# Optimization experiments

Measured on AMD Instinct MI355X. Metric: run time of the kernel, lower is better.

## Reference

```python
import jax, jax.numpy as jnp
import numpy as np

B, S, D = 16, 2048, 1024   # batch, src_len, per-tensor feature dim (input_dim*growth_factor)
OUT = 1024                 # output_dim


def setup_inputs() -> dict:
    key = jax.random.key(0)
    k1, k2, k3, k4, k5, k6 = jax.random.split(key, 6)
    hidden = jax.random.normal(k1, (B, S, D), dtype=jnp.float32)
    encoder_outputs = jax.random.normal(k2, (B, S, D), dtype=jnp.float32)
    c_t = jax.random.normal(k3, (B, D), dtype=jnp.float32)
    # Linear(input_dim*3*growth_factor=3*D, OUT): PyTorch stores weight as [OUT, 3D]
    limit = 1.0 / np.sqrt(3 * D)
    W = jax.random.uniform(k4, (OUT, 3 * D), minval=-limit, maxval=limit, dtype=jnp.float32)
    b = jax.random.uniform(k5, (OUT,), minval=-limit, maxval=limit, dtype=jnp.float32)
    v = jax.random.uniform(k6, (OUT,), dtype=jnp.float32)  # torch.rand -> U[0,1)
    return {"hidden": hidden, "encoder_outputs": encoder_outputs, "c_t": c_t,
            "W": W, "b": b, "v": v}


def reference(hidden, encoder_outputs, c_t, W, b, v):
    # c_t broadcast over src_len; concat on feature dim -> [B, S, 3D]
    c_rep = jnp.broadcast_to(c_t[:, None, :], hidden.shape)
    cat = jnp.concatenate((hidden, c_rep, encoder_outputs), axis=2)
    # energy = relu(cat @ W^T + b): [B, S, OUT]
    energy = jax.nn.relu(jnp.einsum('bsf,of->bso', cat, W) + b)
    # attention = energy @ v: [B, S], then softmax over src_len
    attention = jnp.einsum('bso,o->bs', energy, v)
    return jax.nn.softmax(attention, axis=1)
```

## Files before the change

### kernel.cpp

```cpp
#include <hip/hip_runtime.h>
#include <hip/hip_bf16.h>


typedef __attribute__((ext_vector_type(8))) short short8;
typedef __attribute__((ext_vector_type(4))) float f32x4;
typedef __attribute__((ext_vector_type(8))) unsigned short ushort8v;
typedef __attribute__((ext_vector_type(4))) unsigned short ushort4v;

#define NB 16
#define NS 2048
#define ND 1024
#define NOUT 1024
#define NM (NB * NS)
#define KHE 2048
#define TM 128
#define TN 128
#define BK 32

__device__ __forceinline__ unsigned short bf16_rne(float x) {
    unsigned int u = __float_as_uint(x);
    unsigned int r = (u + 0x7fffu + ((u >> 16) & 1u)) >> 16;
    return (unsigned short)r;
}

__device__ __forceinline__ void gload_lds16(const unsigned short* g, unsigned short* l) {
    __builtin_amdgcn_global_load_lds(
        (const __attribute__((address_space(1))) void*)g,
        (__attribute__((address_space(3))) void*)l, 16, 0, 0);
}

__global__ __launch_bounds__(256) void aconv_k(const float* __restrict__ hidden,
                                               const float* __restrict__ enc,
                                               unsigned short* __restrict__ Abf) {
    size_t c = (size_t)blockIdx.x * 256 + threadIdx.x;
    size_t m = c >> 8;
    int k = (int)(c & 255) * 8;
    const float* src = (k < ND) ? (hidden + m * ND + k) : (enc + m * ND + (k - ND));
    float4 f0 = *(const float4*)src;
    float4 f1 = *(const float4*)(src + 4);
    ushort8v h;
    h[0] = bf16_rne(f0.x); h[1] = bf16_rne(f0.y); h[2] = bf16_rne(f0.z); h[3] = bf16_rne(f0.w);
    h[4] = bf16_rne(f1.x); h[5] = bf16_rne(f1.y); h[6] = bf16_rne(f1.z); h[7] = bf16_rne(f1.w);
    *(ushort8v*)(Abf + m * KHE + k) = h;
}

__global__ __launch_bounds__(256) void wconv_k(const float* __restrict__ W,
                                               unsigned short* __restrict__ Wbf) {
    int idx = blockIdx.x * 256 + threadIdx.x;
    int o = idx >> 9;
    int k = (idx & 511) * 4;
    int off = (k < ND) ? k : (k + ND);
    float4 f = *(const float4*)(W + (size_t)o * 3072 + off);
    ushort4v h;
    h.x = bf16_rne(f.x); h.y = bf16_rne(f.y); h.z = bf16_rne(f.z); h.w = bf16_rne(f.w);
    *(ushort4v*)(Wbf + (size_t)o * KHE + k) = h;
}

__global__ __launch_bounds__(256) void cbias_k(const float* __restrict__ c_t,
                                               const float* __restrict__ W,
                                               const float* __restrict__ bias,
                                               float* __restrict__ cbias) {
    int o = blockIdx.x * 4 + (threadIdx.x >> 6);
    int lane = threadIdx.x & 63;
    const float* w = W + (size_t)o * 3072 + ND;
    float wr[16];
    #pragma unroll
    for (int j = 0; j < 16; ++j) wr[j] = w[lane + j * 64];
    float bo = bias[o];
    for (int b = 0; b < NB; ++b) {
        const float* c = c_t + (size_t)b * ND;
        float s = 0.f;
        #pragma unroll
        for (int j = 0; j < 16; ++j) s = fmaf(c[lane + j * 64], wr[j], s);
        #pragma unroll
        for (int m = 1; m < 64; m <<= 1) s += __shfl_xor(s, m);
        if (lane == 0) cbias[b * NOUT + o] = s + bo;
    }
}

__global__ __launch_bounds__(256) void gemm_att_bf_k(const unsigned short* __restrict__ Abf,
                                                     const unsigned short* __restrict__ Wbf,
                                                     const float* __restrict__ cbias,
                                                     const float* __restrict__ v,
                                                     float* __restrict__ logits) {
    __shared__ unsigned short As[TM * BK] __attribute__((aligned(16)));
    __shared__ unsigned short Bs[TN * BK] __attribute__((aligned(16)));
    __shared__ float rowsum[2][TM];
    __shared__ float cb_s[TN];
    __shared__ float v_s[TN];

    const int tid = threadIdx.x;
    const int ntile = blockIdx.x & 7;
    const int mtile = blockIdx.x >> 3;
    const int m0 = mtile * TM;
    const int o0 = ntile * TN;
    const int batch = m0 >> 11;

    if (tid < TN) {
        cb_s[tid] = cbias[batch * NOUT + o0 + tid];
        v_s[tid] = v[o0 + tid];
    }

    const int wid = tid >> 6;
    const int lane = tid & 63;
    const int wm = (wid & 1) * 64;
    const int wn = (wid >> 1) * 64;

    const int srow = lane >> 2;
    const int scol = (lane & 3) * 8;
    const unsigned short* ag0 = Abf + (size_t)(m0 + wid * 32 + srow) * KHE + scol;
    const unsigned short* ag1 = ag0 + (size_t)16 * KHE;
    const unsigned short* bg0 = Wbf + (size_t)(o0 + wid * 32 + srow) * KHE + scol;
    const unsigned short* bg1 = bg0 + (size_t)16 * KHE;
    unsigned short* al0 = As + (wid * 32) * BK;
    unsigned short* al1 = As + (wid * 32 + 16) * BK;
    unsigned short* bl0 = Bs + (wid * 32) * BK;
    unsigned short* bl1 = Bs + (wid * 32 + 16) * BK;

    f32x4 acc[4][4] = {};

    for (int kt = 0; kt < KHE; kt += BK) {
        gload_lds16(ag0 + kt, al0);
        gload_lds16(ag1 + kt, al1);
        gload_lds16(bg0 + kt, bl0);
        gload_lds16(bg1 + kt, bl1);
        __syncthreads();

        short8 a_frag[4], b_frag[4];
        #pragma unroll
        for (int i = 0; i < 4; ++i)
            a_frag[i] = *(const short8*)(As + (wm + i * 16 + (lane & 15)) * BK + (lane >> 4) * 8);
        #pragma unroll
        for (int j = 0; j < 4; ++j)
            b_frag[j] = *(const short8*)(Bs + (wn + j * 16 + (lane & 15)) * BK + (lane >> 4) * 8);
        #pragma unroll
        for (int i = 0; i < 4; ++i)
            #pragma unroll
            for (int j = 0; j < 4; ++j)
                acc[i][j] = __builtin_amdgcn_mfma_f32_16x16x32_bf16(a_frag[i], b_frag[j],
                                                                    acc[i][j], 0, 0, 0);
        __syncthreads();
    }

    const int col = lane & 15;
    const int q = lane >> 4;
    float vv[4], cbv[4];
    #pragma unroll
    for (int j = 0; j < 4; ++j) {
        int oc = wn + j * 16 + col;
        vv[j] = v_s[oc];
        cbv[j] = cb_s[oc];
    }
    #pragma unroll
    for (int i = 0; i < 4; ++i) {
        #pragma unroll
        for (int r = 0; r < 4; ++r) {
            float s = 0.f;
            #pragma unroll
            for (int j = 0; j < 4; ++j) {
                float e = acc[i][j][r] + cbv[j];
                e = fmaxf(e, 0.f);
                s = fmaf(e, vv[j], s);
            }
            s += __shfl_xor(s, 1);
            s += __shfl_xor(s, 2);
            s += __shfl_xor(s, 4);
            s += __shfl_xor(s, 8);
            if (col == 0) rowsum[wid >> 1][wm + i * 16 + q * 4 + r] = s;
        }
    }
    __syncthreads();
    if (tid < TM) atomicAdd(&logits[m0 + tid], rowsum[0][tid] + rowsum[1][tid]);
}

__global__ __launch_bounds__(256) void gemm_att_k(const float* __restrict__ hidden,
                                                  const float* __restrict__ enc,
                                                  const unsigned short* __restrict__ Wbf,
                                                  const float* __restrict__ Wf,
                                                  const float* __restrict__ cbias,
                                                  const float* __restrict__ v,
                                                  float* __restrict__ logits,
                                                  int use_wbf) {
    __shared__ unsigned short As[TM * BK] __attribute__((aligned(16)));
    __shared__ unsigned short Bs[TN * BK] __attribute__((aligned(16)));
    __shared__ float rowsum[2][TM];
    __shared__ float cb_s[TN];
    __shared__ float v_s[TN];

    const int tid = threadIdx.x;
    const int ntile = blockIdx.x & 7;
    const int mtile = blockIdx.x >> 3;
    const int m0 = mtile * TM;
    const int o0 = ntile * TN;
    const int batch = m0 >> 11;

    if (tid < TN) {
        cb_s[tid] = cbias[batch * NOUT + o0 + tid];
        v_s[tid] = v[o0 + tid];
    }

    const int wid = tid >> 6;
    const int lane = tid & 63;
    const int wm = (wid & 1) * 64;
    const int wn = (wid >> 1) * 64;

    f32x4 acc[4][4] = {};

    for (int kt = 0; kt < KHE; kt += BK) {
        const float* Abase = (kt < ND) ? hidden : enc;
        const int aoff = (kt < ND) ? kt : (kt - ND);
        #pragma unroll
        for (int i = 0; i < 4; ++i) {
            int p = tid + i * 256;
            int row = p >> 3, kc = p & 7;
            float4 f = *(const float4*)(Abase + (size_t)(m0 + row) * ND + aoff + kc * 4);
            ushort4v h;
            h.x = bf16_rne(f.x); h.y = bf16_rne(f.y); h.z = bf16_rne(f.z); h.w = bf16_rne(f.w);
            *(ushort4v*)(As + row * BK + kc * 4) = h;
        }
        if (use_wbf) {
            #pragma unroll
            for (int i = 0; i < 2; ++i) {
                int u = tid + i * 256;
                int ol = u >> 2, kc = u & 3;
                ushort8v w8 = *(const ushort8v*)(Wbf + (size_t)(o0 + ol) * KHE + kt + kc * 8);
                *(ushort8v*)(Bs + ol * BK + kc * 8) = w8;
            }
        } else {
            const int woff = (kt < ND) ? kt : (kt + ND);
            #pragma unroll
            for (int i = 0; i < 4; ++i) {
                int p = tid + i * 256;
                int row = p >> 3, kc = p & 7;
                float4 f = *(const float4*)(Wf + (size_t)(o0 + row) * 3072 + woff + kc * 4);
                ushort4v h;
                h.x = bf16_rne(f.x); h.y = bf16_rne(f.y); h.z = bf16_rne(f.z); h.w = bf16_rne(f.w);
                *(ushort4v*)(Bs + row * BK + kc * 4) = h;
            }
        }
        __syncthreads();

        short8 a_frag[4], b_frag[4];
        #pragma unroll
        for (int i = 0; i < 4; ++i)
            a_frag[i] = *(const short8*)(As + (wm + i * 16 + (lane & 15)) * BK + (lane >> 4) * 8);
        #pragma unroll
        for (int j = 0; j < 4; ++j)
            b_frag[j] = *(const short8*)(Bs + (wn + j * 16 + (lane & 15)) * BK + (lane >> 4) * 8);
        #pragma unroll
        for (int i = 0; i < 4; ++i)
            #pragma unroll
            for (int j = 0; j < 4; ++j)
                acc[i][j] = __builtin_amdgcn_mfma_f32_16x16x32_bf16(a_frag[i], b_frag[j],
                                                                    acc[i][j], 0, 0, 0);
        __syncthreads();
    }

    const int col = lane & 15;
    const int q = lane >> 4;
    float vv[4], cbv[4];
    #pragma unroll
    for (int j = 0; j < 4; ++j) {
        int oc = wn + j * 16 + col;
        vv[j] = v_s[oc];
        cbv[j] = cb_s[oc];
    }
    #pragma unroll
    for (int i = 0; i < 4; ++i) {
        #pragma unroll
        for (int r = 0; r < 4; ++r) {
            float s = 0.f;
            #pragma unroll
            for (int j = 0; j < 4; ++j) {
                float e = acc[i][j][r] + cbv[j];
                e = fmaxf(e, 0.f);
                s = fmaf(e, vv[j], s);
            }
            s += __shfl_xor(s, 1);
            s += __shfl_xor(s, 2);
            s += __shfl_xor(s, 4);
            s += __shfl_xor(s, 8);
            if (col == 0) rowsum[wid >> 1][wm + i * 16 + q * 4 + r] = s;
        }
    }
    __syncthreads();
    if (tid < TM) atomicAdd(&logits[m0 + tid], rowsum[0][tid] + rowsum[1][tid]);
}

__global__ __launch_bounds__(256) void softmax_k(const float* __restrict__ logits,
                                                 float* __restrict__ out) {
    const int b = blockIdx.x;
    const int tid = threadIdx.x;
    const int lane = tid & 63, wid = tid >> 6;
    __shared__ float redmax[4];
    __shared__ float redsum[4];
    const float* L = logits + (size_t)b * NS;
    float x[8];
    float mx = -3.4e38f;
    #pragma unroll
    for (int i = 0; i < 8; ++i) {
        x[i] = L[tid + i * 256];
        mx = fmaxf(mx, x[i]);
    }
    #pragma unroll
    for (int m = 1; m < 64; m <<= 1) mx = fmaxf(mx, __shfl_xor(mx, m));
    if (lane == 0) redmax[wid] = mx;
    __syncthreads();
    mx = fmaxf(fmaxf(redmax[0], redmax[1]), fmaxf(redmax[2], redmax[3]));
    float sum = 0.f;
    #pragma unroll
    for (int i = 0; i < 8; ++i) {
        x[i] = expf(x[i] - mx);
        sum += x[i];
    }
    #pragma unroll
    for (int m = 1; m < 64; m <<= 1) sum += __shfl_xor(sum, m);
    if (lane == 0) redsum[wid] = sum;
    __syncthreads();
    float inv = 1.0f / (redsum[0] + redsum[1] + redsum[2] + redsum[3]);
    #pragma unroll
    for (int i = 0; i < 8; ++i) out[(size_t)b * NS + tid + i * 256] = x[i] * inv;
}

extern "C" void kernel_launch(void* const* d_in, const int* in_sizes, int n_in,
                              void* d_out, int out_size, void* d_ws, size_t ws_size,
                              hipStream_t stream) {
    const float* hidden = (const float*)d_in[0];
    const float* enc    = (const float*)d_in[1];
    const float* c_t    = (const float*)d_in[2];
    const float* W      = (const float*)d_in[3];
    const float* bias   = (const float*)d_in[4];
    const float* v      = (const float*)d_in[5];
    float* out = (float*)d_out;

    char* ws = (char*)d_ws;
    float* logits = (float*)ws;
    float* cbias  = (float*)(ws + 131072);
    unsigned short* Wbf = (unsigned short*)(ws + 196608);
    unsigned short* Abf = (unsigned short*)(ws + 196608 + 4194304);
    const size_t need_wbf = 196608 + (size_t)NOUT * KHE * 2;
    const size_t need_abf = need_wbf + (size_t)NM * KHE * 2;

    hipMemsetAsync(logits, 0, NM * sizeof(float), stream);
    cbias_k<<<NOUT / 4, 256, 0, stream>>>(c_t, W, bias, cbias);

    if (ws_size >= need_abf) {
        wconv_k<<<(NOUT * KHE / 4) / 256, 256, 0, stream>>>(W, Wbf);
        aconv_k<<<(int)(((size_t)NM * KHE / 8) / 256), 256, 0, stream>>>(hidden, enc, Abf);
        gemm_att_bf_k<<<(NM / TM) * (NOUT / TN), 256, 0, stream>>>(Abf, Wbf, cbias, v, logits);
    } else if (ws_size >= need_wbf) {
        wconv_k<<<(NOUT * KHE / 4) / 256, 256, 0, stream>>>(W, Wbf);
        gemm_att_k<<<(NM / TM) * (NOUT / TN), 256, 0, stream>>>(hidden, enc, Wbf, W, cbias, v,
                                                                logits, 1);
    } else {
        gemm_att_k<<<(NM / TM) * (NOUT / TN), 256, 0, stream>>>(hidden, enc, Wbf, W, cbias, v,
                                                                logits, 0);
    }
    softmax_k<<<NB, 256, 0, stream>>>(logits, out);
}
```

Baseline: 495.1 us.

## Fuse prep kernels and double K-tile with XOR-swizzled LDS layout in bf16 GEMM

Merges the memset, c_t bias, weight and activation conversions into a single prep kernel to cut launch overhead. The bf16 GEMM moves from a 32-wide to a 64-wide K tile, which halves the number of barrier pairs per tile. Its LDS layout is XOR-swizzled by row so fragment reads avoid bank conflicts. The larger tile doubles LDS use per block, which may lower occupancy.

```diff
diff --git a/kernel.cpp b/kernel.cpp
--- a/kernel.cpp
+++ b/kernel.cpp
@@ -15,7 +15,12 @@
 #define KHE 2048
 #define TM 128
 #define TN 128
-#define BK 32
+#define BK 64
+
+#define PREP_ACONV 16384
+#define PREP_WCONV 2048
+#define PREP_CBIAS 256
+#define PREP_ZERO 32
 
 __device__ __forceinline__ unsigned short bf16_rne(float x) {
     unsigned int u = __float_as_uint(x);
@@ -29,19 +34,63 @@
         (__attribute__((address_space(3))) void*)l, 16, 0, 0);
 }
 
-__global__ __launch_bounds__(256) void aconv_k(const float* __restrict__ hidden,
-                                               const float* __restrict__ enc,
-                                               unsigned short* __restrict__ Abf) {
-    size_t c = (size_t)blockIdx.x * 256 + threadIdx.x;
-    size_t m = c >> 8;
-    int k = (int)(c & 255) * 8;
-    const float* src = (k < ND) ? (hidden + m * ND + k) : (enc + m * ND + (k - ND));
-    float4 f0 = *(const float4*)src;
-    float4 f1 = *(const float4*)(src + 4);
-    ushort8v h;
-    h[0] = bf16_rne(f0.x); h[1] = bf16_rne(f0.y); h[2] = bf16_rne(f0.z); h[3] = bf16_rne(f0.w);
-    h[4] = bf16_rne(f1.x); h[5] = bf16_rne(f1.y); h[6] = bf16_rne(f1.z); h[7] = bf16_rne(f1.w);
-    *(ushort8v*)(Abf + m * KHE + k) = h;
+__global__ __launch_bounds__(256) void prep_k(const float* __restrict__ hidden,
+                                              const float* __restrict__ enc,
+                                              const float* __restrict__ c_t,
+                                              const float* __restrict__ W,
+                                              const float* __restrict__ bias,
+                                              unsigned short* __restrict__ Abf,
+                                              unsigned short* __restrict__ Wbf,
+                                              float* __restrict__ cbias,
+                                              float* __restrict__ logits) {
+    const int bid = blockIdx.x;
+    const int tid = threadIdx.x;
+    if (bid < PREP_ACONV) {
+        size_t c = (size_t)bid * 256 + tid;
+        size_t m = c >> 7;
+        int k = (int)(c & 127) * 16;
+        const float* src = (k < ND) ? (hidden + m * ND + k) : (enc + m * ND + (k - ND));
+        float4 f0 = ((const float4*)src)[0];
+        float4 f1 = ((const float4*)src)[1];
+        float4 f2 = ((const float4*)src)[2];
+        float4 f3 = ((const float4*)src)[3];
+        ushort8v h0, h1;
+        h0[0] = bf16_rne(f0.x); h0[1] = bf16_rne(f0.y); h0[2] = bf16_rne(f0.z); h0[3] = bf16_rne(f0.w);
+        h0[4] = bf16_rne(f1.x); h0[5] = bf16_rne(f1.y); h0[6] = bf16_rne(f1.z); h0[7] = bf16_rne(f1.w);
+        h1[0] = bf16_rne(f2.x); h1[1] = bf16_rne(f2.y); h1[2] = bf16_rne(f2.z); h1[3] = bf16_rne(f2.w);
+        h1[4] = bf16_rne(f3.x); h1[5] = bf16_rne(f3.y); h1[6] = bf16_rne(f3.z); h1[7] = bf16_rne(f3.w);
+        *(ushort8v*)(Abf + m * KHE + k) = h0;
+        *(ushort8v*)(Abf + m * KHE + k + 8) = h1;
+    } else if (bid < PREP_ACONV + PREP_WCONV) {
+        int idx = (bid - PREP_ACONV) * 256 + tid;
+        int o = idx >> 9;
+        int k = (idx & 511) * 4;
+        int off = (k < ND) ? k : (k + ND);
+        float4 f = *(const float4*)(W + (size_t)o * 3072 + off);
+        ushort4v h;
+        h.x = bf16_rne(f.x); h.y = bf16_rne(f.y); h.z = bf16_rne(f.z); h.w = bf16_rne(f.w);
+        *(ushort4v*)(Wbf + (size_t)o * KHE + k) = h;
+    } else if (bid < PREP_ACONV + PREP_WCONV + PREP_CBIAS) {
+        int o = (bid - PREP_ACONV - PREP_WCONV) * 4 + (tid >> 6);
+        int lane = tid & 63;
+        const float* w = W + (size_t)o * 3072 + ND;
+        float wr[16];
+        #pragma unroll
+        for (int j = 0; j < 16; ++j) wr[j] = w[lane + j * 64];
+        float bo = bias[o];
+        for (int b = 0; b < NB; ++b) {
+            const float* cc = c_t + (size_t)b * ND;
+            float s = 0.f;
+            #pragma unroll
+            for (int j = 0; j < 16; ++j) s = fmaf(cc[lane + j * 64], wr[j], s);
+            #pragma unroll
+            for (int m = 1; m < 64; m <<= 1) s += __shfl_xor(s, m);
+            if (lane == 0) cbias[b * NOUT + o] = s + bo;
+        }
+    } else {
+        int idx = (bid - PREP_ACONV - PREP_WCONV - PREP_CBIAS) * 256 + tid;
+        ((float4*)logits)[idx] = make_float4(0.f, 0.f, 0.f, 0.f);
+    }
 }
 
 __global__ __launch_bounds__(256) void wconv_k(const float* __restrict__ W,
@@ -106,39 +155,44 @@
     const int wm = (wid & 1) * 64;
     const int wn = (wid >> 1) * 64;
 
-    const int srow = lane >> 2;
-    const int scol = (lane & 3) * 8;
-    const unsigned short* ag0 = Abf + (size_t)(m0 + wid * 32 + srow) * KHE + scol;
-    const unsigned short* ag1 = ag0 + (size_t)16 * KHE;
-    const unsigned short* bg0 = Wbf + (size_t)(o0 + wid * 32 + srow) * KHE + scol;
-    const unsigned short* bg1 = bg0 + (size_t)16 * KHE;
-    unsigned short* al0 = As + (wid * 32) * BK;
-    unsigned short* al1 = As + (wid * 32 + 16) * BK;
-    unsigned short* bl0 = Bs + (wid * 32) * BK;
-    unsigned short* bl1 = Bs + (wid * 32 + 16) * BK;
+    const int srow = lane >> 3;
+    const int schunk = (lane & 7) ^ srow;
+    const unsigned short* agb = Abf + (size_t)(m0 + wid * 32 + srow) * KHE + schunk * 8;
+    const unsigned short* bgb = Wbf + (size_t)(o0 + wid * 32 + srow) * KHE + schunk * 8;
+    unsigned short* alb = As + (wid * 32) * BK;
+    unsigned short* blb = Bs + (wid * 32) * BK;
 
     f32x4 acc[4][4] = {};
 
     for (int kt = 0; kt < KHE; kt += BK) {
-        gload_lds16(ag0 + kt, al0);
-        gload_lds16(ag1 + kt, al1);
-        gload_lds16(bg0 + kt, bl0);
-        gload_lds16(bg1 + kt, bl1);
+        #pragma unroll
+        for (int t = 0; t < 4; ++t) {
+            gload_lds16(agb + (size_t)(t * 8) * KHE + kt, alb + (t * 8) * BK);
+            gload_lds16(bgb + (size_t)(t * 8) * KHE + kt, blb + (t * 8) * BK);
+        }
         __syncthreads();
 
-        short8 a_frag[4], b_frag[4];
-        #pragma unroll
-        for (int i = 0; i < 4; ++i)
-            a_frag[i] = *(const short8*)(As + (wm + i * 16 + (lane & 15)) * BK + (lane >> 4) * 8);
-        #pragma unroll
-        for (int j = 0; j < 4; ++j)
-            b_frag[j] = *(const short8*)(Bs + (wn + j * 16 + (lane & 15)) * BK + (lane >> 4) * 8);
-        #pragma unroll
-        for (int i = 0; i < 4; ++i)
-            #pragma unroll
-            for (int j = 0; j < 4; ++j)
-                acc[i][j] = __builtin_amdgcn_mfma_f32_16x16x32_bf16(a_frag[i], b_frag[j],
-                                                                    acc[i][j], 0, 0, 0);
+        #pragma unroll
+        for (int s = 0; s < 2; ++s) {
+            const int cbase = s * 4 + (lane >> 4);
+            short8 a_frag[4], b_frag[4];
+            #pragma unroll
+            for (int i = 0; i < 4; ++i) {
+                int row = wm + i * 16 + (lane & 15);
+                a_frag[i] = *(const short8*)(As + row * BK + ((cbase ^ (row & 7)) * 8));
+            }
+            #pragma unroll
+            for (int j = 0; j < 4; ++j) {
+                int row = wn + j * 16 + (lane & 15);
+                b_frag[j] = *(const short8*)(Bs + row * BK + ((cbase ^ (row & 7)) * 8));
+            }
+            #pragma unroll
+            for (int i = 0; i < 4; ++i)
+                #pragma unroll
+                for (int j = 0; j < 4; ++j)
+                    acc[i][j] = __builtin_amdgcn_mfma_f32_16x16x32_bf16(a_frag[i], b_frag[j],
+                                                                        acc[i][j], 0, 0, 0);
+        }
         __syncthreads();
     }
 
@@ -181,8 +235,8 @@
                                                   const float* __restrict__ v,
                                                   float* __restrict__ logits,
                                                   int use_wbf) {
-    __shared__ unsigned short As[TM * BK] __attribute__((aligned(16)));
-    __shared__ unsigned short Bs[TN * BK] __attribute__((aligned(16)));
+    __shared__ unsigned short As[TM * 32] __attribute__((aligned(16)));
+    __shared__ unsigned short Bs[TN * 32] __attribute__((aligned(16)));
     __shared__ float rowsum[2][TM];
     __shared__ float cb_s[TN];
     __shared__ float v_s[TN];
@@ -206,7 +260,7 @@
 
     f32x4 acc[4][4] = {};
 
-    for (int kt = 0; kt < KHE; kt += BK) {
+    for (int kt = 0; kt < KHE; kt += 32) {
         const float* Abase = (kt < ND) ? hidden : enc;
         const int aoff = (kt < ND) ? kt : (kt - ND);
         #pragma unroll
@@ -216,7 +270,7 @@
             float4 f = *(const float4*)(Abase + (size_t)(m0 + row) * ND + aoff + kc * 4);
             ushort4v h;
             h.x = bf16_rne(f.x); h.y = bf16_rne(f.y); h.z = bf16_rne(f.z); h.w = bf16_rne(f.w);
-            *(ushort4v*)(As + row * BK + kc * 4) = h;
+            *(ushort4v*)(As + row * 32 + kc * 4) = h;
         }
         if (use_wbf) {
             #pragma unroll
@@ -224,7 +278,7 @@
                 int u = tid + i * 256;
                 int ol = u >> 2, kc = u & 3;
                 ushort8v w8 = *(const ushort8v*)(Wbf + (size_t)(o0 + ol) * KHE + kt + kc * 8);
-                *(ushort8v*)(Bs + ol * BK + kc * 8) = w8;
+                *(ushort8v*)(Bs + ol * 32 + kc * 8) = w8;
             }
         } else {
             const int woff = (kt < ND) ? kt : (kt + ND);
@@ -235,7 +289,7 @@
                 float4 f = *(const float4*)(Wf + (size_t)(o0 + row) * 3072 + woff + kc * 4);
                 ushort4v h;
                 h.x = bf16_rne(f.x); h.y = bf16_rne(f.y); h.z = bf16_rne(f.z); h.w = bf16_rne(f.w);
-                *(ushort4v*)(Bs + row * BK + kc * 4) = h;
+                *(ushort4v*)(Bs + row * 32 + kc * 4) = h;
             }
         }
         __syncthreads();
@@ -243,10 +297,10 @@
         short8 a_frag[4], b_frag[4];
         #pragma unroll
         for (int i = 0; i < 4; ++i)
-            a_frag[i] = *(const short8*)(As + (wm + i * 16 + (lane & 15)) * BK + (lane >> 4) * 8);
+            a_frag[i] = *(const short8*)(As + (wm + i * 16 + (lane & 15)) * 32 + (lane >> 4) * 8);
         #pragma unroll
         for (int j = 0; j < 4; ++j)
-            b_frag[j] = *(const short8*)(Bs + (wn + j * 16 + (lane & 15)) * BK + (lane >> 4) * 8);
+            b_frag[j] = *(const short8*)(Bs + (wn + j * 16 + (lane & 15)) * 32 + (lane >> 4) * 8);
         #pragma unroll
         for (int i = 0; i < 4; ++i)
             #pragma unroll
@@ -341,18 +395,19 @@
     const size_t need_wbf = 196608 + (size_t)NOUT * KHE * 2;
     const size_t need_abf = need_wbf + (size_t)NM * KHE * 2;
 
-    hipMemsetAsync(logits, 0, NM * sizeof(float), stream);
-    cbias_k<<<NOUT / 4, 256, 0, stream>>>(c_t, W, bias, cbias);
-
     if (ws_size >= need_abf) {
-        wconv_k<<<(NOUT * KHE / 4) / 256, 256, 0, stream>>>(W, Wbf);
-        aconv_k<<<(int)(((size_t)NM * KHE / 8) / 256), 256, 0, stream>>>(hidden, enc, Abf);
+        prep_k<<<PREP_ACONV + PREP_WCONV + PREP_CBIAS + PREP_ZERO, 256, 0, stream>>>(
+            hidden, enc, c_t, W, bias, Abf, Wbf, cbias, logits);
         gemm_att_bf_k<<<(NM / TM) * (NOUT / TN), 256, 0, stream>>>(Abf, Wbf, cbias, v, logits);
     } else if (ws_size >= need_wbf) {
+        hipMemsetAsync(logits, 0, NM * sizeof(float), stream);
+        cbias_k<<<NOUT / 4, 256, 0, stream>>>(c_t, W, bias, cbias);
         wconv_k<<<(NOUT * KHE / 4) / 256, 256, 0, stream>>>(W, Wbf);
         gemm_att_k<<<(NM / TM) * (NOUT / TN), 256, 0, stream>>>(hidden, enc, Wbf, W, cbias, v,
                                                                 logits, 1);
     } else {
+        hipMemsetAsync(logits, 0, NM * sizeof(float), stream);
+        cbias_k<<<NOUT / 4, 256, 0, stream>>>(c_t, W, bias, cbias);
         gemm_att_k<<<(NM / TM) * (NOUT / TN), 256, 0, stream>>>(hidden, enc, Wbf, W, cbias, v,
                                                                 logits, 0);
     }
```

After: 481.7 us. 2.7% less time.
